# Kernel optimization log

Hardware: AMD Instinct MI355X
Metric: run time of the kernel (lower is better)

The kernel has to match this reference:

```python
import jax, jax.numpy as jnp
import numpy as np

B, S, D = 32, 576, 768
G = 24  # sqrt(S)
TEMP = 0.01


def grid_sample_bilinear_zeros(img, grid):
    # img: (B,C,H,W), grid: (B,Hg,Wg,2) in [-1,1]; torch F.grid_sample,
    # mode='bilinear', padding_mode='zeros', align_corners=False
    Bn, C, H, W = img.shape
    gx, gy = grid[..., 0], grid[..., 1]
    ix = ((gx + 1.0) * W - 1.0) * 0.5
    iy = ((gy + 1.0) * H - 1.0) * 0.5
    x0 = jnp.floor(ix); y0 = jnp.floor(iy)
    x1 = x0 + 1.0;      y1 = y0 + 1.0
    wx1 = ix - x0; wx0 = 1.0 - wx1
    wy1 = iy - y0; wy0 = 1.0 - wy1

    def gather(xi, yi):
        valid = (xi >= 0) & (xi <= W - 1) & (yi >= 0) & (yi <= H - 1)
        xc = jnp.clip(xi, 0, W - 1).astype(jnp.int32)
        yc = jnp.clip(yi, 0, H - 1).astype(jnp.int32)
        vals = jax.vmap(lambda im, y, x: im[:, y, x])(img, yc, xc)  # (B,C,Hg,Wg)
        return vals * valid.astype(img.dtype)[:, None, :, :]

    return (gather(x0, y0) * (wx0 * wy0)[:, None]
            + gather(x1, y0) * (wx1 * wy0)[:, None]
            + gather(x0, y1) * (wx0 * wy1)[:, None]
            + gather(x1, y1) * (wx1 * wy1)[:, None])


def key_finder_net(h, W1, b1, W2, b2, W3, b3):
    # fc1 -> relu -> fc2 -> relu -> fc3 -> tanh
    h = jax.nn.relu(h @ W1 + b1)
    h = jax.nn.relu(h @ W2 + b2)
    return jnp.tanh(h @ W3 + b3)


def setup_inputs() -> dict:
    key = jax.random.key(0)
    ks = jax.random.split(key, 16)
    sd = 1.0 / np.sqrt(D)
    inp = {
        'x': jax.random.normal(ks[0], (B, S, D), dtype=jnp.float32),
        'indices': jax.random.randint(ks[1], (B, S), 0, S),
        'Wq': jax.random.normal(ks[2], (D, D), dtype=jnp.float32) * sd,
        'bq': jnp.zeros((D,), jnp.float32),
        'Wk': jax.random.normal(ks[3], (D, D), dtype=jnp.float32) * sd,
        'bk': jnp.zeros((D,), jnp.float32),
        'Wv': jax.random.normal(ks[4], (D, D), dtype=jnp.float32) * sd,
        'bv': jnp.zeros((D,), jnp.float32),
        'W1': jax.random.normal(ks[5], (2 * D, 60), dtype=jnp.float32) / np.sqrt(2 * D),
        'b1': jnp.zeros((60,), jnp.float32),
        'W2': jax.random.normal(ks[6], (60, 60), dtype=jnp.float32) / np.sqrt(60),
        'b2': jnp.zeros((60,), jnp.float32),
        'W3': jax.random.normal(ks[7], (60, 2), dtype=jnp.float32) / np.sqrt(60),
        'b3': jnp.zeros((2,), jnp.float32),
    }
    return inp


def reference(x, indices, Wq, bq, Wk, bk, Wv, bv, W1, b1, W2, b2, W3, b3):
    q = x @ Wq + bq  # (B,S,D)
    k = x @ Wk + bk
    v = x @ Wv + bv

    sample = key_finder_net(jnp.concatenate([q, k], axis=2), W1, b1, W2, b2, W3, b3)  # (B,S,2)
    # torch: cat((sample_x, sample_y), dim=1).reshape(B,G,G,2)
    flat = jnp.concatenate([sample[:, :, 0], sample[:, :, 1]], axis=1)  # (B,2S)
    grid = flat.reshape(B, G, G, 2)

    k_img = jnp.transpose(k, (0, 2, 1)).reshape(B, D, G, G)
    v_img = jnp.transpose(v, (0, 2, 1)).reshape(B, D, G, G)

    sk = grid_sample_bilinear_zeros(k_img, grid)  # (B,D,G,G)
    sv = grid_sample_bilinear_zeros(v_img, grid)
    sampled_key = jnp.transpose(sk.reshape(B, D, G * G), (0, 2, 1))   # (B,S,D)
    sampled_value = jnp.transpose(sv.reshape(B, D, G * G), (0, 2, 1))

    scores = jnp.sum(q * sampled_key, axis=-1)  # (B,S)
    return jax.nn.sigmoid(TEMP * scores)[..., None] * sampled_value
```

## Files before the change

kernel.cpp:

```cpp
#include <hip/hip_runtime.h>

typedef _Float16 f16;
typedef _Float16 f16x8 __attribute__((ext_vector_type(8)));
typedef _Float16 f16x4 __attribute__((ext_vector_type(4)));
typedef float f32x4 __attribute__((ext_vector_type(4)));

constexpr int NB = 32, NS = 576, ND = 768, NG = 24;
constexpr int M_TOT = NB * NS;
constexpr int N_TOT = 3 * ND;

__global__ __launch_bounds__(256) void cast_w_t_kernel(const float* __restrict__ Wq,
                                                       const float* __restrict__ Wk,
                                                       const float* __restrict__ Wv,
                                                       f16* __restrict__ WT) {
  __shared__ float tile[64][65];
  int bt = blockIdx.x;
  int ntile = bt / 12, ktile = bt % 12;
  const float* src = (ntile < 12) ? Wq : ((ntile < 24) ? Wk : Wv);
  int n0 = (ntile % 12) * 64, k0 = ktile * 64;
  int cc = threadIdx.x & 63, rr = threadIdx.x >> 6;
#pragma unroll
  for (int i = 0; i < 16; i++) {
    int k = rr + i * 4;
    tile[cc][k] = src[(size_t)(k0 + k) * ND + n0 + cc];
  }
  __syncthreads();
#pragma unroll
  for (int i = 0; i < 16; i++) {
    int n = rr + i * 4;
    WT[(size_t)(ntile * 64 + n) * ND + k0 + cc] = (f16)tile[n][cc];
  }
}

__global__ __launch_bounds__(256) void wcT_kernel(const float* __restrict__ Wq,
                                                  const float* __restrict__ Wk,
                                                  const float* __restrict__ bq,
                                                  const float* __restrict__ bk,
                                                  const float* __restrict__ W1,
                                                  const float* __restrict__ b1,
                                                  f16* __restrict__ WcT_hi,
                                                  f16* __restrict__ WcT_lo,
                                                  float* __restrict__ bc) {
  if (blockIdx.x == 768) {
    int c = threadIdx.x;
    if (c < 60) {
      float acc = b1[c];
      for (int j = 0; j < ND; j++)
        acc += bq[j] * W1[j * 60 + c] + bk[j] * W1[(ND + j) * 60 + c];
      bc[c] = acc;
    }
    return;
  }
  __shared__ float part[4][64];
  int r = blockIdx.x;
  int wave = threadIdx.x >> 6, lane = threadIdx.x & 63;
  int c = (lane < 60) ? lane : 59;
  const float* wq = Wq + (size_t)r * ND;
  const float* wk = Wk + (size_t)r * ND;
  float acc = 0.f;
  int j0 = wave * 192;
  for (int j = j0; j < j0 + 192; j++)
    acc += wq[j] * W1[j * 60 + c] + wk[j] * W1[(ND + j) * 60 + c];
  part[wave][lane] = acc;
  __syncthreads();
  if (wave == 0 && lane < 60) {
    float v = part[0][lane] + part[1][lane] + part[2][lane] + part[3][lane];
    f16 hi = (f16)v;
    WcT_hi[(size_t)lane * ND + r] = hi;
    WcT_lo[(size_t)lane * ND + r] = (f16)(v - (float)hi);
  }
}

__global__ __launch_bounds__(256) void z1_fused_kernel(const float* __restrict__ x,
                                                       const f16* __restrict__ WcT_hi,
                                                       const f16* __restrict__ WcT_lo,
                                                       const float* __restrict__ bc,
                                                       const float* __restrict__ W2,
                                                       const float* __restrict__ b2,
                                                       const float* __restrict__ W3,
                                                       const float* __restrict__ b3,
                                                       f16* __restrict__ xb,
                                                       float* __restrict__ coords) {
  __shared__ float red[3][16][64];
  __shared__ float htile[16][60];
  int wave = threadIdx.x >> 6, lane = threadIdx.x & 63;
  int q = lane >> 4, r16 = lane & 15;
  int m0 = blockIdx.x * 16;
  int k0 = wave * 192;
  const float* xr = x + (size_t)(m0 + r16) * ND + k0;
  f16* xbr = xb + (size_t)(m0 + r16) * ND + k0;

  f32x4 acc[4];
#pragma unroll
  for (int nf = 0; nf < 4; nf++) acc[nf] = 0.f;

  for (int kk = 0; kk < 192; kk += 32) {
    int ko = kk + q * 8;
    float4 v0 = *(const float4*)(xr + ko);
    float4 v1 = *(const float4*)(xr + ko + 4);
    f16x8 a_hi, a_lo;
    float xv[8] = {v0.x, v0.y, v0.z, v0.w, v1.x, v1.y, v1.z, v1.w};
#pragma unroll
    for (int j = 0; j < 8; j++) {
      f16 h = (f16)xv[j];
      a_hi[j] = h;
      a_lo[j] = (f16)(xv[j] - (float)h);
    }
    *(f16x8*)(xbr + ko) = a_hi;
    f16x8 b_hi[4], b_lo[4];
#pragma unroll
    for (int nf = 0; nf < 4; nf++) {
      size_t off = (size_t)(nf * 16 + r16) * ND + k0 + ko;
      b_hi[nf] = *(const f16x8*)(WcT_hi + off);
      b_lo[nf] = *(const f16x8*)(WcT_lo + off);
    }
#pragma unroll
    for (int nf = 0; nf < 4; nf++) {
      acc[nf] = __builtin_amdgcn_mfma_f32_16x16x32_f16(a_hi, b_hi[nf], acc[nf], 0, 0, 0);
      acc[nf] = __builtin_amdgcn_mfma_f32_16x16x32_f16(a_lo, b_hi[nf], acc[nf], 0, 0, 0);
      acc[nf] = __builtin_amdgcn_mfma_f32_16x16x32_f16(a_hi, b_lo[nf], acc[nf], 0, 0, 0);
    }
  }

  if (wave > 0) {
#pragma unroll
    for (int nf = 0; nf < 4; nf++)
#pragma unroll
      for (int r = 0; r < 4; r++) red[wave - 1][nf * 4 + r][lane] = acc[nf][r];
  }
  __syncthreads();
  if (wave == 0) {
#pragma unroll
    for (int nf = 0; nf < 4; nf++) {
      int col = nf * 16 + r16;
      if (col < 60) {
        float bcv = bc[col];
#pragma unroll
        for (int r = 0; r < 4; r++) {
          float v = acc[nf][r] + red[0][nf * 4 + r][lane] + red[1][nf * 4 + r][lane]
                  + red[2][nf * 4 + r][lane] + bcv;
          htile[q * 4 + r][col] = fmaxf(v, 0.f);
        }
      }
    }
  }
  __syncthreads();

  int c = (lane < 60) ? lane : 59;
  float b2v = b2[c];
  float w30 = W3[c * 2 + 0], w31 = W3[c * 2 + 1];
#pragma unroll
  for (int rr = 0; rr < 4; rr++) {
    int row = wave * 4 + rr;
    float acc2 = b2v;
    for (int j = 0; j < 60; j++) acc2 = fmaf(htile[row][j], W2[j * 60 + c], acc2);
    float h2 = fmaxf(acc2, 0.f);
    float p0 = (lane < 60) ? h2 * w30 : 0.f;
    float p1 = (lane < 60) ? h2 * w31 : 0.f;
#pragma unroll
    for (int o = 32; o > 0; o >>= 1) { p0 += __shfl_down(p0, o); p1 += __shfl_down(p1, o); }
    if (lane == 0) {
      float s0 = tanhf(p0 + b3[0]);
      float s1 = tanhf(p1 + b3[1]);
      int m = m0 + row;
      int b = m / NS, s = m % NS;
      float* cb = coords + (size_t)b * (2 * NS);
      cb[(s >> 1) * 2 + (s & 1)] = s0;
      cb[(288 + (s >> 1)) * 2 + (s & 1)] = s1;
    }
  }
}

__device__ __forceinline__ void async_copy16(const f16* g, f16* l) {
  __builtin_amdgcn_global_load_lds((const __attribute__((address_space(1))) void*)g,
                                   (__attribute__((address_space(3))) void*)l, 16, 0, 0);
}

__global__ __launch_bounds__(256) void gemm_kernel(const f16* __restrict__ A,
                                                   const f16* __restrict__ Bt,
                                                   const float* __restrict__ bq,
                                                   const float* __restrict__ bk,
                                                   const float* __restrict__ bv,
                                                   f16* __restrict__ C) {
  constexpr int BM = 128, BK = 64;
  __shared__ __align__(16) f16 sA[BM * BK];
  __shared__ __align__(16) f16 sB[BM * BK];

  int bm = blockIdx.x % (M_TOT / BM);
  int bn = blockIdx.x / (M_TOT / BM);
  int tid = threadIdx.x;
  int wave = tid >> 6, lane = tid & 63;
  int wm = (wave >> 1) * 64, wn = (wave & 1) * 64;
  int m0 = bm * BM, n0 = bn * BM;

  int srow = tid >> 3;
  int gchunk = ((tid & 7) ^ (srow & 7)) * 8;

  f32x4 acc[4][4];
#pragma unroll
  for (int i = 0; i < 4; i++)
#pragma unroll
    for (int j = 0; j < 4; j++) acc[i][j] = 0.f;

  int q = lane >> 4, r16 = lane & 15;

  for (int kk = 0; kk < ND; kk += BK) {
#pragma unroll
    for (int ps = 0; ps < 4; ps++) {
      async_copy16(A + (size_t)(m0 + ps * 32 + srow) * ND + kk + gchunk, sA + ps * 2048 + tid * 8);
      async_copy16(Bt + (size_t)(n0 + ps * 32 + srow) * ND + kk + gchunk, sB + ps * 2048 + tid * 8);
    }
    __syncthreads();

#pragma unroll
    for (int h = 0; h < 2; h++) {
      f16x8 aF[4], bF[4];
#pragma unroll
      for (int mt = 0; mt < 4; mt++) {
        int R = wm + mt * 16 + r16;
        aF[mt] = *(const f16x8*)(sA + R * 64 + (((h * 4 + q) ^ (R & 7)) * 8));
      }
#pragma unroll
      for (int nt = 0; nt < 4; nt++) {
        int R = wn + nt * 16 + r16;
        bF[nt] = *(const f16x8*)(sB + R * 64 + (((h * 4 + q) ^ (R & 7)) * 8));
      }
#pragma unroll
      for (int mt = 0; mt < 4; mt++)
#pragma unroll
        for (int nt = 0; nt < 4; nt++)
          acc[mt][nt] = __builtin_amdgcn_mfma_f32_16x16x32_f16(bF[nt], aF[mt], acc[mt][nt], 0, 0, 0);
    }
    __syncthreads();
  }

#pragma unroll
  for (int mt = 0; mt < 4; mt++) {
    int gm = m0 + wm + mt * 16 + r16;
#pragma unroll
    for (int nt = 0; nt < 4; nt++) {
      int gn0 = n0 + wn + nt * 16 + q * 4;
      const float* bp = (gn0 < ND) ? (bq + gn0)
                      : ((gn0 < 2 * ND) ? (bk + gn0 - ND) : (bv + gn0 - 2 * ND));
      float4 bias = *(const float4*)bp;
      f16x4 o;
      o[0] = (f16)(acc[mt][nt][0] + bias.x);
      o[1] = (f16)(acc[mt][nt][1] + bias.y);
      o[2] = (f16)(acc[mt][nt][2] + bias.z);
      o[3] = (f16)(acc[mt][nt][3] + bias.w);
      *(f16x4*)(C + (size_t)gm * N_TOT + gn0) = o;
    }
  }
}

__global__ __launch_bounds__(256) void sample_kernel(const f16* __restrict__ qkv,
                                                     const float* __restrict__ coords,
                                                     float* __restrict__ out) {
  int wave = threadIdx.x >> 6, t = threadIdx.x & 63;
  int idx = blockIdx.x * 4 + wave;
  int b = idx / NS, p = idx % NS;

  float gx = coords[(size_t)b * (2 * NS) + p * 2 + 0];
  float gy = coords[(size_t)b * (2 * NS) + p * 2 + 1];
  float ix = ((gx + 1.f) * (float)NG - 1.f) * 0.5f;
  float iy = ((gy + 1.f) * (float)NG - 1.f) * 0.5f;
  float x0f = floorf(ix), y0f = floorf(iy);
  float wx1 = ix - x0f, wx0 = 1.f - wx1;
  float wy1 = iy - y0f, wy0 = 1.f - wy1;
  int x0 = (int)x0f, y0 = (int)y0f, x1 = x0 + 1, y1 = y0 + 1;
  bool vx0 = (x0 >= 0) & (x0 <= NG - 1), vx1 = (x1 >= 0) & (x1 <= NG - 1);
  bool vy0 = (y0 >= 0) & (y0 <= NG - 1), vy1 = (y1 >= 0) & (y1 <= NG - 1);
  int cx0 = min(max(x0, 0), NG - 1), cx1 = min(max(x1, 0), NG - 1);
  int cy0 = min(max(y0, 0), NG - 1), cy1 = min(max(y1, 0), NG - 1);
  float w00 = wx0 * wy0 * ((vx0 && vy0) ? 1.f : 0.f);
  float w10 = wx1 * wy0 * ((vx1 && vy0) ? 1.f : 0.f);
  float w01 = wx0 * wy1 * ((vx0 && vy1) ? 1.f : 0.f);
  float w11 = wx1 * wy1 * ((vx1 && vy1) ? 1.f : 0.f);

  size_t base = (size_t)b * NS;
  const f16* r00 = qkv + (base + cy0 * NG + cx0) * N_TOT;
  const f16* r10 = qkv + (base + cy0 * NG + cx1) * N_TOT;
  const f16* r01 = qkv + (base + cy1 * NG + cx0) * N_TOT;
  const f16* r11 = qkv + (base + cy1 * NG + cx1) * N_TOT;
  const f16* qr  = qkv + (base + p) * N_TOT;

  int d0 = t * 12;
  float partial = 0.f;
  float outv[12];
#pragma unroll
  for (int ch = 0; ch < 3; ch++) {
    int d = d0 + ch * 4;
    f16x4 k00 = *(const f16x4*)(r00 + ND + d);
    f16x4 k10 = *(const f16x4*)(r10 + ND + d);
    f16x4 k01 = *(const f16x4*)(r01 + ND + d);
    f16x4 k11 = *(const f16x4*)(r11 + ND + d);
    f16x4 v00 = *(const f16x4*)(r00 + 2 * ND + d);
    f16x4 v10 = *(const f16x4*)(r10 + 2 * ND + d);
    f16x4 v01 = *(const f16x4*)(r01 + 2 * ND + d);
    f16x4 v11 = *(const f16x4*)(r11 + 2 * ND + d);
    f16x4 qv  = *(const f16x4*)(qr + d);
#pragma unroll
    for (int j = 0; j < 4; j++) {
      float sk = w00 * (float)k00[j] + w10 * (float)k10[j]
               + w01 * (float)k01[j] + w11 * (float)k11[j];
      float sv = w00 * (float)v00[j] + w10 * (float)v10[j]
               + w01 * (float)v01[j] + w11 * (float)v11[j];
      partial = fmaf((float)qv[j], sk, partial);
      outv[ch * 4 + j] = sv;
    }
  }
#pragma unroll
  for (int o = 32; o > 0; o >>= 1) partial += __shfl_down(partial, o);
  float score = __shfl(partial, 0);
  float sig = 1.f / (1.f + expf(-0.01f * score));
  float* orow = out + (size_t)(base + p) * ND;
#pragma unroll
  for (int ch = 0; ch < 3; ch++) {
    float4 st;
    st.x = sig * outv[ch * 4 + 0]; st.y = sig * outv[ch * 4 + 1];
    st.z = sig * outv[ch * 4 + 2]; st.w = sig * outv[ch * 4 + 3];
    *(float4*)(orow + d0 + ch * 4) = st;
  }
}

extern "C" void kernel_launch(void* const* d_in, const int* in_sizes, int n_in,
                              void* d_out, int out_size, void* d_ws, size_t ws_size,
                              hipStream_t stream) {
  const float* x  = (const float*)d_in[0];
  const float* Wq = (const float*)d_in[2];
  const float* bq = (const float*)d_in[3];
  const float* Wk = (const float*)d_in[4];
  const float* bk = (const float*)d_in[5];
  const float* Wv = (const float*)d_in[6];
  const float* bv = (const float*)d_in[7];
  const float* W1 = (const float*)d_in[8];
  const float* b1 = (const float*)d_in[9];
  const float* W2 = (const float*)d_in[10];
  const float* b2 = (const float*)d_in[11];
  const float* W3 = (const float*)d_in[12];
  const float* b3 = (const float*)d_in[13];
  float* out = (float*)d_out;

  char* ws = (char*)d_ws;
  f16*   xb     = (f16*)(ws);
  f16*   WT     = (f16*)(ws + 28311552);
  f16*   qkv    = (f16*)(ws + 31850496);
  f16*   WcT_hi = (f16*)(ws + 31850496);
  f16*   WcT_lo = (f16*)(ws + 31948800);
  float* bc     = (float*)(ws + 116969472);
  float* coords = (float*)(ws + 121393408);

  cast_w_t_kernel<<<dim3(432), dim3(256), 0, stream>>>(Wq, Wk, Wv, WT);
  wcT_kernel<<<dim3(769), dim3(256), 0, stream>>>(Wq, Wk, bq, bk, W1, b1, WcT_hi, WcT_lo, bc);
  z1_fused_kernel<<<dim3(M_TOT / 16), dim3(256), 0, stream>>>(x, WcT_hi, WcT_lo, bc,
                                                              W2, b2, W3, b3, xb, coords);
  gemm_kernel<<<dim3((M_TOT / 128) * (N_TOT / 128)), dim3(256), 0, stream>>>(xb, WT, bq, bk, bv, qkv);
  sample_kernel<<<dim3(M_TOT / 4), dim3(256), 0, stream>>>(qkv, coords, out);
  (void)in_sizes; (void)n_in; (void)out_size; (void)ws_size;
}
```

Measured before the change: 349.5 us.

## Switch QKV GEMM to 32x32x16 MFMA and remap sample blocks by XCD

The QKV projection GEMM now uses the 32x32x16 f16 MFMA with 2x2 tiles per wave instead of 4x4 tiles of 16x16x32. This cuts the number of MFMA issues and fragment loads per wave, and the epilogue is rewritten for the 32x32 output layout. The sample kernel also remaps block indices so that consecutive blocks on the same XCD (blockIdx mod 8) handle the same batch, which is meant to improve L2 locality for gathers. The remap assumes 8 XCDs and exactly 32*576/4 blocks.

Measured after the change: 349.0 us. About the same (-0.1%).

```diff
diff --git a/kernel.cpp b/kernel.cpp
--- a/kernel.cpp
+++ b/kernel.cpp
@@ -4,6 +4,7 @@
 typedef _Float16 f16x8 __attribute__((ext_vector_type(8)));
 typedef _Float16 f16x4 __attribute__((ext_vector_type(4)));
 typedef float f32x4 __attribute__((ext_vector_type(4)));
+typedef float f32x16 __attribute__((ext_vector_type(16)));
 
 constexpr int NB = 32, NS = 576, ND = 768, NG = 24;
 constexpr int M_TOT = NB * NS;
@@ -196,13 +197,13 @@
   int srow = tid >> 3;
   int gchunk = ((tid & 7) ^ (srow & 7)) * 8;
 
-  f32x4 acc[4][4];
-#pragma unroll
-  for (int i = 0; i < 4; i++)
-#pragma unroll
-    for (int j = 0; j < 4; j++) acc[i][j] = 0.f;
-
-  int q = lane >> 4, r16 = lane & 15;
+  f32x16 acc[2][2];
+#pragma unroll
+  for (int i = 0; i < 2; i++)
+#pragma unroll
+    for (int j = 0; j < 2; j++) acc[i][j] = 0.f;
+
+  int r32 = lane & 31, q2 = lane >> 5;
 
   for (int kk = 0; kk < ND; kk += BK) {
 #pragma unroll
@@ -213,42 +214,45 @@
     __syncthreads();
 
 #pragma unroll
-    for (int h = 0; h < 2; h++) {
-      f16x8 aF[4], bF[4];
-#pragma unroll
-      for (int mt = 0; mt < 4; mt++) {
-        int R = wm + mt * 16 + r16;
-        aF[mt] = *(const f16x8*)(sA + R * 64 + (((h * 4 + q) ^ (R & 7)) * 8));
+    for (int ks = 0; ks < 4; ks++) {
+      f16x8 aF[2], bF[2];
+#pragma unroll
+      for (int mt = 0; mt < 2; mt++) {
+        int R = wm + mt * 32 + r32;
+        aF[mt] = *(const f16x8*)(sA + R * 64 + (((ks * 2 + q2) ^ (R & 7)) * 8));
       }
 #pragma unroll
-      for (int nt = 0; nt < 4; nt++) {
-        int R = wn + nt * 16 + r16;
-        bF[nt] = *(const f16x8*)(sB + R * 64 + (((h * 4 + q) ^ (R & 7)) * 8));
+      for (int nt = 0; nt < 2; nt++) {
+        int R = wn + nt * 32 + r32;
+        bF[nt] = *(const f16x8*)(sB + R * 64 + (((ks * 2 + q2) ^ (R & 7)) * 8));
       }
 #pragma unroll
-      for (int mt = 0; mt < 4; mt++)
-#pragma unroll
-        for (int nt = 0; nt < 4; nt++)
-          acc[mt][nt] = __builtin_amdgcn_mfma_f32_16x16x32_f16(bF[nt], aF[mt], acc[mt][nt], 0, 0, 0);
+      for (int mt = 0; mt < 2; mt++)
+#pragma unroll
+        for (int nt = 0; nt < 2; nt++)
+          acc[mt][nt] = __builtin_amdgcn_mfma_f32_32x32x16_f16(bF[nt], aF[mt], acc[mt][nt], 0, 0, 0);
     }
     __syncthreads();
   }
 
 #pragma unroll
-  for (int mt = 0; mt < 4; mt++) {
-    int gm = m0 + wm + mt * 16 + r16;
-#pragma unroll
-    for (int nt = 0; nt < 4; nt++) {
-      int gn0 = n0 + wn + nt * 16 + q * 4;
-      const float* bp = (gn0 < ND) ? (bq + gn0)
-                      : ((gn0 < 2 * ND) ? (bk + gn0 - ND) : (bv + gn0 - 2 * ND));
-      float4 bias = *(const float4*)bp;
-      f16x4 o;
-      o[0] = (f16)(acc[mt][nt][0] + bias.x);
-      o[1] = (f16)(acc[mt][nt][1] + bias.y);
-      o[2] = (f16)(acc[mt][nt][2] + bias.z);
-      o[3] = (f16)(acc[mt][nt][3] + bias.w);
-      *(f16x4*)(C + (size_t)gm * N_TOT + gn0) = o;
+  for (int mt = 0; mt < 2; mt++) {
+    int gm = m0 + wm + mt * 32 + r32;
+#pragma unroll
+    for (int nt = 0; nt < 2; nt++) {
+#pragma unroll
+      for (int g = 0; g < 4; g++) {
+        int gn0 = n0 + wn + nt * 32 + 8 * g + 4 * q2;
+        const float* bp = (gn0 < ND) ? (bq + gn0)
+                        : ((gn0 < 2 * ND) ? (bk + gn0 - ND) : (bv + gn0 - 2 * ND));
+        float4 bias = *(const float4*)bp;
+        f16x4 o;
+        o[0] = (f16)(acc[mt][nt][4 * g + 0] + bias.x);
+        o[1] = (f16)(acc[mt][nt][4 * g + 1] + bias.y);
+        o[2] = (f16)(acc[mt][nt][4 * g + 2] + bias.z);
+        o[3] = (f16)(acc[mt][nt][4 * g + 3] + bias.w);
+        *(f16x4*)(C + (size_t)gm * N_TOT + gn0) = o;
+      }
     }
   }
 }
@@ -257,8 +261,10 @@
                                                      const float* __restrict__ coords,
                                                      float* __restrict__ out) {
   int wave = threadIdx.x >> 6, t = threadIdx.x & 63;
-  int idx = blockIdx.x * 4 + wave;
-  int b = idx / NS, p = idx % NS;
+  int x8 = blockIdx.x & 7;
+  int i = blockIdx.x >> 3;
+  int b = x8 * 4 + (i / 144);
+  int p = (i % 144) * 4 + wave;
 
   float gx = coords[(size_t)b * (2 * NS) + p * 2 + 0];
   float gy = coords[(size_t)b * (2 * NS) + p * 2 + 1];
```

## Double-buffer GEMM LDS tiles and remap sample blocks across XCDs

Applied to the files above, without the earlier changes.

The QKV GEMM now keeps two LDS buffers for A and B and issues the async global-to-LDS loads for the next K tile before computing on the current one. This overlaps memory latency with MFMA work, at the cost of doubling LDS use per block, which may lower occupancy. The sample kernel also remaps blockIdx so that the 8 round-robin dispatch slots (likely the XCDs) each handle a contiguous group of 4 batches, which is meant to improve L2 locality for the qkv gathers.

Result: slower. 365.2 us (+4.5%).

```diff
diff --git a/kernel.cpp b/kernel.cpp
--- a/kernel.cpp
+++ b/kernel.cpp
@@ -183,8 +183,8 @@
                                                    const float* __restrict__ bv,
                                                    f16* __restrict__ C) {
   constexpr int BM = 128, BK = 64;
-  __shared__ __align__(16) f16 sA[BM * BK];
-  __shared__ __align__(16) f16 sB[BM * BK];
+  __shared__ __align__(16) f16 sA[2][BM * BK];
+  __shared__ __align__(16) f16 sB[2][BM * BK];
 
   int bm = blockIdx.x % (M_TOT / BM);
   int bn = blockIdx.x / (M_TOT / BM);
@@ -204,26 +204,39 @@
 
   int q = lane >> 4, r16 = lane & 15;
 
-  for (int kk = 0; kk < ND; kk += BK) {
-#pragma unroll
-    for (int ps = 0; ps < 4; ps++) {
-      async_copy16(A + (size_t)(m0 + ps * 32 + srow) * ND + kk + gchunk, sA + ps * 2048 + tid * 8);
-      async_copy16(Bt + (size_t)(n0 + ps * 32 + srow) * ND + kk + gchunk, sB + ps * 2048 + tid * 8);
-    }
-    __syncthreads();
-
+#pragma unroll
+  for (int ps = 0; ps < 4; ps++) {
+    async_copy16(A + (size_t)(m0 + ps * 32 + srow) * ND + gchunk, &sA[0][ps * 2048 + tid * 8]);
+    async_copy16(Bt + (size_t)(n0 + ps * 32 + srow) * ND + gchunk, &sB[0][ps * 2048 + tid * 8]);
+  }
+  __syncthreads();
+
+  for (int i = 0; i < ND / BK; i++) {
+    int cur = i & 1;
+    if (i + 1 < ND / BK) {
+      int kk = (i + 1) * BK;
+#pragma unroll
+      for (int ps = 0; ps < 4; ps++) {
+        async_copy16(A + (size_t)(m0 + ps * 32 + srow) * ND + kk + gchunk,
+                     &sA[1 - cur][ps * 2048 + tid * 8]);
+        async_copy16(Bt + (size_t)(n0 + ps * 32 + srow) * ND + kk + gchunk,
+                     &sB[1 - cur][ps * 2048 + tid * 8]);
+      }
+    }
+    const f16* pA = sA[cur];
+    const f16* pB = sB[cur];
 #pragma unroll
     for (int h = 0; h < 2; h++) {
       f16x8 aF[4], bF[4];
 #pragma unroll
       for (int mt = 0; mt < 4; mt++) {
         int R = wm + mt * 16 + r16;
-        aF[mt] = *(const f16x8*)(sA + R * 64 + (((h * 4 + q) ^ (R & 7)) * 8));
+        aF[mt] = *(const f16x8*)(pA + R * 64 + (((h * 4 + q) ^ (R & 7)) * 8));
       }
 #pragma unroll
       for (int nt = 0; nt < 4; nt++) {
         int R = wn + nt * 16 + r16;
-        bF[nt] = *(const f16x8*)(sB + R * 64 + (((h * 4 + q) ^ (R & 7)) * 8));
+        bF[nt] = *(const f16x8*)(pB + R * 64 + (((h * 4 + q) ^ (R & 7)) * 8));
       }
 #pragma unroll
       for (int mt = 0; mt < 4; mt++)
@@ -257,8 +270,10 @@
                                                      const float* __restrict__ coords,
                                                      float* __restrict__ out) {
   int wave = threadIdx.x >> 6, t = threadIdx.x & 63;
-  int idx = blockIdx.x * 4 + wave;
-  int b = idx / NS, p = idx % NS;
+  int x8 = blockIdx.x & 7;
+  int i = blockIdx.x >> 3;
+  int b = x8 * 4 + (i / 144);
+  int p = (i % 144) * 4 + wave;
 
   float gx = coords[(size_t)b * (2 * NS) + p * 2 + 0];
   float gy = coords[(size_t)b * (2 * NS) + p * 2 + 1];
```
